# Optimization experiments

Hardware: AMD Instinct MI355X
Metric: run time of the kernel (lower is better)

The kernel has to match this reference:

```python
import jax, jax.numpy as jnp
import numpy as np

B, S, E, H, D = 4, 2048, 1024, 8, 128
EPS = 1e-5


def _ln(x, g, b):
    m = jnp.mean(x, axis=-1, keepdims=True)
    v = jnp.mean((x - m) ** 2, axis=-1, keepdims=True)
    return (x - m) * jax.lax.rsqrt(v + EPS) * g + b


def _xavier(k, shape, fan_in, fan_out):
    lim = float(np.sqrt(6.0 / (fan_in + fan_out)))
    return jax.random.uniform(k, shape, jnp.float32, -lim, lim)


def setup_inputs() -> dict:
    key = jax.random.key(0)
    ks = jax.random.split(key, 10)
    return {
        "x": jax.random.normal(ks[0], (B, S, E), jnp.float32),
        # embedding_to_z: Linear(E, H*D); stored as [E, H*D] for x @ W
        "W_ez": _xavier(ks[1], (E, H * D), E, H * D),
        "b_ez": jnp.zeros((H * D,), jnp.float32),
        "U_h": _xavier(ks[2], (H, D, D), D, D),
        "U_z": _xavier(ks[3], (H, D, D), D, D),
        "b_u": jnp.zeros((H, D), jnp.float32),
        "out_shaper": _xavier(ks[4], (H, D, D), D, D),
        # shared per-step state LayerNorm
        "lns_g": jnp.ones((D,), jnp.float32),
        "lns_b": jnp.zeros((D,), jnp.float32),
        # per-head FFN: LayerNorm(D) -> Linear(D,D) -> GELU -> Linear(D,E)
        "ff_ln_g": jnp.ones((H, D), jnp.float32),
        "ff_ln_b": jnp.zeros((H, D), jnp.float32),
        "ff_W1": _xavier(ks[5], (H, D, D), D, D),
        "ff_b1": jnp.zeros((H, D), jnp.float32),
        "ff_W2": _xavier(ks[6], (H, D, E), D, E),
        "ff_b2": jnp.zeros((H, E), jnp.float32),
        # layer_attention_weights: Linear(E, 1)
        "w_att": _xavier(ks[7], (E,), E, 1),
        "b_att": jnp.zeros((), jnp.float32),
        # output LayerNorm
        "lno_g": jnp.ones((E,), jnp.float32),
        "lno_b": jnp.zeros((E,), jnp.float32),
    }


def reference(x, W_ez, b_ez, U_h, U_z, b_u, out_shaper, lns_g, lns_b,
              ff_ln_g, ff_ln_b, ff_W1, ff_b1, ff_W2, ff_b2,
              w_att, b_att, lno_g, lno_b):
    b, s, _ = x.shape
    h, d = U_h.shape[0], U_h.shape[1]
    # z tokens: [B,S,H,D]
    z = jnp.tanh((x @ W_ez + b_ez).reshape(b, s, h, d))
    # torch.einsum('bhd,hdd->bhd') takes the DIAGONAL of the second operand
    uh_diag = jnp.einsum('hii->hi', U_h)          # [H,D]
    uz_diag = jnp.einsum('hii->hi', U_z)          # [H,D]
    os_diag = jnp.einsum('hii->hi', out_shaper)   # [H,D]

    def step(h_prev, z_t):
        # h_prev, z_t: [B,H,D]
        u = jax.nn.sigmoid(h_prev * uh_diag + z_t * uz_diag + b_u)
        h_new = u * h_prev + (1.0 - u) * z_t
        h_new = _ln(h_new, lns_g, lns_b)
        return h_new, h_new

    h0 = jnp.zeros((b, h, d), x.dtype)
    _, states = jax.lax.scan(step, h0, jnp.swapaxes(z, 0, 1))  # [S,B,H,D]
    states = jnp.swapaxes(states, 0, 1)                         # [B,S,H,D]

    shaped = states * os_diag                                   # diag einsum
    hln = _ln(shaped, ff_ln_g, ff_ln_b)                         # per-head LN
    h1 = jax.nn.gelu(jnp.einsum('bshd,hde->bshe', hln, ff_W1) + ff_b1,
                     approximate=False)                         # [B,S,H,D]
    ff_out = jnp.einsum('bshd,hde->bshe', h1, ff_W2) + ff_b2    # [B,S,H,E]

    scores = jax.nn.softmax(jnp.einsum('bshe,e->bsh', ff_out, w_att) + b_att,
                            axis=2)                             # over heads
    weighted = jnp.einsum('bshe,bsh->bse', ff_out, scores)      # [B,S,E]
    return _ln(weighted, lno_g, lno_b)
```

## Files before the change

kernel.cpp:

```cpp
#include <hip/hip_runtime.h>
#include <hip/hip_bf16.h>
#include <math.h>

#define BB 4
#define SS 2048
#define EE 1024
#define HH 8
#define DD 128
#define BSR (BB*SS)
#define HD  (HH*DD)
#define LNEPS 1e-5f
#define LOG2E 1.4426950408889634f

typedef __attribute__((ext_vector_type(8))) short bf16x8;
typedef __attribute__((ext_vector_type(4))) float f32x4;

__device__ __forceinline__ ushort f2bf(float f) {
    union { float f; unsigned u; } c{f};
    unsigned r = c.u + 0x7fff + ((c.u >> 16) & 1);
    return (ushort)(r >> 16);
}
__device__ __forceinline__ float bf2f(ushort b) {
    union { unsigned u; float f; } c{(unsigned)b << 16};
    return c.f;
}

typedef __attribute__((address_space(1))) const unsigned int GUI;
typedef __attribute__((address_space(3))) unsigned int LUI;
__device__ __forceinline__ void gl_lds16(const ushort* g, ushort* l) {
    __builtin_amdgcn_global_load_lds((GUI*)g, (LUI*)l, 16, 0, 0);
}

__global__ __launch_bounds__(256)
void prep_k(const float* __restrict__ W2, const float* __restrict__ w_att,
            const float* __restrict__ b2, const float* __restrict__ b_att,
            const float* __restrict__ Uh, const float* __restrict__ Uz,
            const float* __restrict__ Os,
            float* __restrict__ q, float* __restrict__ c,
            float* __restrict__ uh_d, float* __restrict__ uz_d,
            float* __restrict__ os_d)
{
    const int gid  = blockIdx.x * 256 + threadIdx.x;
    const int wave = gid >> 6, lane = gid & 63;
    if (wave < HD) {
        const float* wp = W2 + (size_t)wave * EE;
        float p = 0.f;
        for (int e = lane; e < EE; e += 64) p = fmaf(wp[e], w_att[e], p);
        #pragma unroll
        for (int off = 32; off > 0; off >>= 1) p += __shfl_xor(p, off, 64);
        if (lane == 0) {
            q[wave] = p;
            const int h = wave >> 7, d = wave & 127;
            uh_d[wave] = Uh[(size_t)h*DD*DD + (size_t)d*DD + d];
            uz_d[wave] = Uz[(size_t)h*DD*DD + (size_t)d*DD + d];
            os_d[wave] = Os[(size_t)h*DD*DD + (size_t)d*DD + d];
        }
    } else if (wave < HD + HH) {
        const int h = wave - HD;
        const float* bp = b2 + (size_t)h * EE;
        float p = 0.f;
        for (int e = lane; e < EE; e += 64) p = fmaf(bp[e], w_att[e], p);
        #pragma unroll
        for (int off = 32; off > 0; off >>= 1) p += __shfl_xor(p, off, 64);
        if (lane == 0) c[h] = p + b_att[0];
    }
}

__global__ __launch_bounds__(256)
void convx2_k(const float* __restrict__ x,
              ushort* __restrict__ hi, ushort* __restrict__ lo)
{
    const size_t idx = ((size_t)blockIdx.x * 256 + threadIdx.x) * 4;
    const float4 v = *(const float4*)(x + idx);
    ushort4 oh, ol;
    oh.x = f2bf(v.x); ol.x = f2bf(v.x - bf2f(oh.x));
    oh.y = f2bf(v.y); ol.y = f2bf(v.y - bf2f(oh.y));
    oh.z = f2bf(v.z); ol.z = f2bf(v.z - bf2f(oh.z));
    oh.w = f2bf(v.w); ol.w = f2bf(v.w - bf2f(oh.w));
    *(ushort4*)(hi + idx) = oh;
    *(ushort4*)(lo + idx) = ol;
}

__global__ __launch_bounds__(256)
void convT2_k(const float* __restrict__ W,
              ushort* __restrict__ Wth, ushort* __restrict__ Wtl)
{
    __shared__ float tile[32][33];
    const int k0 = blockIdx.x * 32, n0 = blockIdx.y * 32;
    const int tx = threadIdx.x & 31, ty = threadIdx.x >> 5;
    #pragma unroll
    for (int i = 0; i < 4; ++i)
        tile[ty + i*8][tx] = W[(size_t)(k0 + ty + i*8) * 1024 + n0 + tx];
    __syncthreads();
    #pragma unroll
    for (int i = 0; i < 4; ++i) {
        const float v = tile[tx][ty + i*8];
        const ushort h = f2bf(v);
        Wth[(size_t)(n0 + ty + i*8) * 1024 + k0 + tx] = h;
        Wtl[(size_t)(n0 + ty + i*8) * 1024 + k0 + tx] = f2bf(v - bf2f(h));
    }
}

__global__ __launch_bounds__(256)
void convT_k(const float* __restrict__ W, ushort* __restrict__ Wt)
{
    __shared__ float tile[32][33];
    const int k0 = blockIdx.x * 32, n0 = blockIdx.y * 32;
    const int tx = threadIdx.x & 31, ty = threadIdx.x >> 5;
    #pragma unroll
    for (int i = 0; i < 4; ++i)
        tile[ty + i*8][tx] = W[(size_t)(k0 + ty + i*8) * 1024 + n0 + tx];
    __syncthreads();
    #pragma unroll
    for (int i = 0; i < 4; ++i)
        Wt[(size_t)(n0 + ty + i*8) * 1024 + k0 + tx] = f2bf(tile[tx][ty + i*8]);
}

__global__ __launch_bounds__(256)
void gemm_mfma_hp(const ushort* __restrict__ Ah, const ushort* __restrict__ Al,
                  const ushort* __restrict__ Bh, const ushort* __restrict__ Bl,
                  float* __restrict__ C, const float* __restrict__ bias)
{
    __shared__ ushort AsmH[128*32], AsmL[128*32];
    __shared__ ushort BsmH[128*32], BsmL[128*32];
    const int t = threadIdx.x, lane = t & 63, w = t >> 6;
    const int wr = w >> 1, wc = w & 1;
    const int row0 = blockIdx.x * 128, col0 = blockIdx.y * 128;

    const int lr = lane >> 2;
    const int lc = (lane & 3) ^ (lr & 3);
    const size_t aoff0 = (size_t)(row0 +      w*16 + lr) * 1024 + lc*8;
    const size_t aoff1 = (size_t)(row0 + 64 + w*16 + lr) * 1024 + lc*8;
    const size_t boff0 = (size_t)(col0 +      w*16 + lr) * 1024 + lc*8;
    const size_t boff1 = (size_t)(col0 + 64 + w*16 + lr) * 1024 + lc*8;
    ushort* lds0 = (ushort*)nullptr;
    (void)lds0;
    ushort* AH0 = AsmH + (     w*16) * 32;  ushort* AH1 = AsmH + (64 + w*16) * 32;
    ushort* AL0 = AsmL + (     w*16) * 32;  ushort* AL1 = AsmL + (64 + w*16) * 32;
    ushort* BH0 = BsmH + (     w*16) * 32;  ushort* BH1 = BsmH + (64 + w*16) * 32;
    ushort* BL0 = BsmL + (     w*16) * 32;  ushort* BL1 = BsmL + (64 + w*16) * 32;

    f32x4 acc[4][4];
    #pragma unroll
    for (int i = 0; i < 4; ++i)
        #pragma unroll
        for (int j = 0; j < 4; ++j) acc[i][j] = (f32x4){0.f,0.f,0.f,0.f};

    const int quad = lane >> 4;
    const int fr   = lane & 15;
    const int fchk = (quad ^ (lane & 3)) * 8;

    for (int k0 = 0; k0 < 1024; k0 += 32) {
        __syncthreads();
        gl_lds16(Ah + aoff0 + k0, AH0);
        gl_lds16(Ah + aoff1 + k0, AH1);
        gl_lds16(Bh + boff0 + k0, BH0);
        gl_lds16(Bh + boff1 + k0, BH1);
        gl_lds16(Al + aoff0 + k0, AL0);
        gl_lds16(Al + aoff1 + k0, AL1);
        gl_lds16(Bl + boff0 + k0, BL0);
        gl_lds16(Bl + boff1 + k0, BL1);
        __syncthreads();

        bf16x8 afh[4], afl[4], bfh[4], bfl[4];
        #pragma unroll
        for (int i = 0; i < 4; ++i) {
            const int ra = (wr*64 + i*16 + fr) * 32 + fchk;
            afh[i] = *(const bf16x8*)(AsmH + ra);
            afl[i] = *(const bf16x8*)(AsmL + ra);
            const int rb = (wc*64 + i*16 + fr) * 32 + fchk;
            bfh[i] = *(const bf16x8*)(BsmH + rb);
            bfl[i] = *(const bf16x8*)(BsmL + rb);
        }
        #pragma unroll
        for (int i = 0; i < 4; ++i)
            #pragma unroll
            for (int j = 0; j < 4; ++j) {
                acc[i][j] = __builtin_amdgcn_mfma_f32_16x16x32_bf16(
                    afh[i], bfl[j], acc[i][j], 0, 0, 0);
                acc[i][j] = __builtin_amdgcn_mfma_f32_16x16x32_bf16(
                    afl[i], bfh[j], acc[i][j], 0, 0, 0);
                acc[i][j] = __builtin_amdgcn_mfma_f32_16x16x32_bf16(
                    afh[i], bfh[j], acc[i][j], 0, 0, 0);
            }
    }

    float colv[4];
    #pragma unroll
    for (int tj = 0; tj < 4; ++tj)
        colv[tj] = bias[col0 + wc*64 + tj*16 + fr];
    #pragma unroll
    for (int ti = 0; ti < 4; ++ti)
        #pragma unroll
        for (int i = 0; i < 4; ++i) {
            const int row = row0 + wr*64 + ti*16 + quad*4 + i;
            #pragma unroll
            for (int tj = 0; tj < 4; ++tj) {
                const int col = col0 + wc*64 + tj*16 + fr;
                C[(size_t)row*1024 + col] = tanhf(acc[ti][tj][i] + colv[tj]);
            }
        }
}

__global__ __launch_bounds__(256)
void gemm_mfma(const ushort* __restrict__ A, const ushort* __restrict__ Bt,
               float* __restrict__ C,
               const float* __restrict__ scores, const float* __restrict__ b2)
{
    __shared__ ushort Asm[128*32];
    __shared__ ushort Bsm[128*32];
    const int t = threadIdx.x, lane = t & 63, w = t >> 6;
    const int wr = w >> 1, wc = w & 1;
    const int row0 = blockIdx.x * 128, col0 = blockIdx.y * 128;

    const int lr = lane >> 2;
    const int lc = (lane & 3) ^ (lr & 3);
    const ushort* Ag0 = A  + (size_t)(row0 +      w*16 + lr) * 1024 + lc*8;
    const ushort* Ag1 = A  + (size_t)(row0 + 64 + w*16 + lr) * 1024 + lc*8;
    const ushort* Bg0 = Bt + (size_t)(col0 +      w*16 + lr) * 1024 + lc*8;
    const ushort* Bg1 = Bt + (size_t)(col0 + 64 + w*16 + lr) * 1024 + lc*8;
    ushort* Al0 = Asm + (     w*16) * 32;
    ushort* Al1 = Asm + (64 + w*16) * 32;
    ushort* Bl0 = Bsm + (     w*16) * 32;
    ushort* Bl1 = Bsm + (64 + w*16) * 32;

    f32x4 acc[4][4];
    #pragma unroll
    for (int i = 0; i < 4; ++i)
        #pragma unroll
        for (int j = 0; j < 4; ++j) acc[i][j] = (f32x4){0.f,0.f,0.f,0.f};

    const int quad = lane >> 4;
    const int fr   = lane & 15;
    const int fchk = (quad ^ (lane & 3)) * 8;

    for (int k0 = 0; k0 < 1024; k0 += 32) {
        __syncthreads();
        gl_lds16(Ag0 + k0, Al0);
        gl_lds16(Ag1 + k0, Al1);
        gl_lds16(Bg0 + k0, Bl0);
        gl_lds16(Bg1 + k0, Bl1);
        __syncthreads();

        bf16x8 af[4], bf[4];
        #pragma unroll
        for (int i = 0; i < 4; ++i) {
            af[i] = *(const bf16x8*)(Asm + (wr*64 + i*16 + fr)*32 + fchk);
            bf[i] = *(const bf16x8*)(Bsm + (wc*64 + i*16 + fr)*32 + fchk);
        }
        #pragma unroll
        for (int i = 0; i < 4; ++i)
            #pragma unroll
            for (int j = 0; j < 4; ++j)
                acc[i][j] = __builtin_amdgcn_mfma_f32_16x16x32_bf16(
                    af[i], bf[j], acc[i][j], 0, 0, 0);
    }

    float b2v[4][HH];
    #pragma unroll
    for (int tj = 0; tj < 4; ++tj) {
        const int col = col0 + wc*64 + tj*16 + fr;
        #pragma unroll
        for (int h = 0; h < HH; ++h) b2v[tj][h] = b2[(size_t)h*EE + col];
    }
    #pragma unroll
    for (int ti = 0; ti < 4; ++ti)
        #pragma unroll
        for (int i = 0; i < 4; ++i) {
            const int row = row0 + wr*64 + ti*16 + quad*4 + i;
            float sc[HH];
            #pragma unroll
            for (int h = 0; h < HH; ++h) sc[h] = scores[row*HH + h];
            #pragma unroll
            for (int tj = 0; tj < 4; ++tj) {
                const int col = col0 + wc*64 + tj*16 + fr;
                float bb = 0.f;
                #pragma unroll
                for (int h = 0; h < HH; ++h) bb = fmaf(sc[h], b2v[tj][h], bb);
                C[(size_t)row*1024 + col] = acc[ti][tj][i] + bb;
            }
        }
}

__global__ __launch_bounds__(256)
void gemm_k(const float* __restrict__ A, int lda, int aOff,
            const float* __restrict__ Bm, int ldb, int bOff,
            float* __restrict__ C, int ldc, int cOff,
            int K,
            const float* __restrict__ bias, int biasOff)
{
    const int zb = blockIdx.z;
    const float* Ab = A  + (size_t)zb * aOff;
    const float* Bb = Bm + (size_t)zb * bOff;
    float*       Cb = C  + (size_t)zb * cOff;
    const float* biasb = bias + (size_t)zb * biasOff;
    const int row0 = blockIdx.x * 128;
    const int col0 = blockIdx.y * 128;

    __shared__ float Asm[8][128];
    __shared__ float Bsm[8][128];

    const int t  = threadIdx.x;
    const int tx = t & 15, ty = t >> 4;
    const int am = t >> 1, ak = (t & 1) * 4;
    const int bk = t >> 5, bn = (t & 31) * 4;

    float acc[8][8];
    #pragma unroll
    for (int i = 0; i < 8; ++i)
        #pragma unroll
        for (int j = 0; j < 8; ++j) acc[i][j] = 0.f;

    for (int k0 = 0; k0 < K; k0 += 8) {
        const float4 av = *(const float4*)(Ab + (size_t)(row0 + am) * lda + k0 + ak);
        const float4 bv = *(const float4*)(Bb + (size_t)(k0 + bk) * ldb + col0 + bn);
        __syncthreads();
        Asm[ak+0][am] = av.x; Asm[ak+1][am] = av.y;
        Asm[ak+2][am] = av.z; Asm[ak+3][am] = av.w;
        *(float4*)&Bsm[bk][bn] = bv;
        __syncthreads();
        #pragma unroll
        for (int kk = 0; kk < 8; ++kk) {
            float a[8], b[8];
            *(float4*)&a[0] = *(const float4*)&Asm[kk][ty*8];
            *(float4*)&a[4] = *(const float4*)&Asm[kk][ty*8+4];
            *(float4*)&b[0] = *(const float4*)&Bsm[kk][tx*8];
            *(float4*)&b[4] = *(const float4*)&Bsm[kk][tx*8+4];
            #pragma unroll
            for (int i = 0; i < 8; ++i)
                #pragma unroll
                for (int j = 0; j < 8; ++j)
                    acc[i][j] = fmaf(a[i], b[j], acc[i][j]);
        }
    }

    #pragma unroll
    for (int i = 0; i < 8; ++i) {
        const int r = row0 + ty*8 + i;
        float outv[8];
        #pragma unroll
        for (int j = 0; j < 8; ++j) {
            const int cidx = col0 + tx*8 + j;
            float v = acc[i][j] + biasb[cidx];
            v = 0.5f * v * (1.f + erff(v * 0.70710678118654752f));
            outv[j] = v;
        }
        *(float4*)(Cb + (size_t)r*ldc + col0 + tx*8)     = *(float4*)&outv[0];
        *(float4*)(Cb + (size_t)r*ldc + col0 + tx*8 + 4) = *(float4*)&outv[4];
    }
}

__device__ __forceinline__ float dpp_add(float x, const int ctrl) {
    int y;
    switch (ctrl) {
        case 0x111: y = __builtin_amdgcn_update_dpp(0, __float_as_int(x), 0x111, 0xf, 0xf, true); break;
        case 0x112: y = __builtin_amdgcn_update_dpp(0, __float_as_int(x), 0x112, 0xf, 0xf, true); break;
        case 0x114: y = __builtin_amdgcn_update_dpp(0, __float_as_int(x), 0x114, 0xf, 0xf, true); break;
        case 0x118: y = __builtin_amdgcn_update_dpp(0, __float_as_int(x), 0x118, 0xf, 0xf, true); break;
        case 0x142: y = __builtin_amdgcn_update_dpp(0, __float_as_int(x), 0x142, 0xf, 0xf, true); break;
        default:    y = __builtin_amdgcn_update_dpp(0, __float_as_int(x), 0x143, 0xf, 0xf, true); break;
    }
    return x + __int_as_float(y);
}

__device__ __forceinline__ float wave_sum64(float x) {
    x = dpp_add(x, 0x111);
    x = dpp_add(x, 0x112);
    x = dpp_add(x, 0x114);
    x = dpp_add(x, 0x118);
    x = dpp_add(x, 0x142);
    x = dpp_add(x, 0x143);
    return __int_as_float(__builtin_amdgcn_readlane(__float_as_int(x), 63));
}

__global__ __launch_bounds__(64)
void scan_k(const float* __restrict__ z,
            const float* __restrict__ uh_d, const float* __restrict__ uz_d,
            const float* __restrict__ b_u,
            const float* __restrict__ lns_g, const float* __restrict__ lns_b,
            float* __restrict__ states)
{
    const int bh = blockIdx.x;
    const int b = bh >> 3, h = bh & 7;
    const int lane = threadIdx.x;
    const int d0 = lane, d1 = lane + 64;

    const float uhn0 = -uh_d[h*DD + d0] * LOG2E, uhn1 = -uh_d[h*DD + d1] * LOG2E;
    const float uzn0 = -uz_d[h*DD + d0] * LOG2E, uzn1 = -uz_d[h*DD + d1] * LOG2E;
    const float bun0 = -b_u [h*DD + d0] * LOG2E, bun1 = -b_u [h*DD + d1] * LOG2E;
    const float g0  = lns_g[d0], g1 = lns_g[d1];
    const float be0 = lns_b[d0], be1 = lns_b[d1];

    const float* zp = z      + ((size_t)b * SS * HH + h) * DD;
    float*       sp = states + ((size_t)b * SS * HH + h) * DD;

    float hp0 = 0.f, hp1 = 0.f;
    const int CH = 8;
    float zc0[CH], zc1[CH], pr0[CH], pr1[CH];
    #pragma unroll
    for (int i = 0; i < CH; ++i) {
        zc0[i] = zp[(size_t)i*HD + d0];
        zc1[i] = zp[(size_t)i*HD + d1];
    }
    #pragma unroll
    for (int i = 0; i < CH; ++i) {
        pr0[i] = fmaf(zc0[i], uzn0, bun0);
        pr1[i] = fmaf(zc1[i], uzn1, bun1);
    }

    for (int s0 = 0; s0 < SS; s0 += CH) {
        float zn0[CH], zn1[CH];
        if (s0 + CH < SS) {
            #pragma unroll
            for (int i = 0; i < CH; ++i) {
                zn0[i] = zp[(size_t)(s0+CH+i)*HD + d0];
                zn1[i] = zp[(size_t)(s0+CH+i)*HD + d1];
            }
        } else {
            #pragma unroll
            for (int i = 0; i < CH; ++i) { zn0[i] = 0.f; zn1[i] = 0.f; }
        }
        #pragma unroll
        for (int i = 0; i < CH; ++i) {
            const float z0 = zc0[i], z1 = zc1[i];
            const float e0 = __builtin_amdgcn_exp2f(fmaf(hp0, uhn0, pr0[i]));
            const float e1 = __builtin_amdgcn_exp2f(fmaf(hp1, uhn1, pr1[i]));
            const float d0v = hp0 - z0;
            const float d1v = hp1 - z1;
            const float u0 = __builtin_amdgcn_rcpf(1.f + e0);
            const float u1 = __builtin_amdgcn_rcpf(1.f + e1);
            const float hn0 = fmaf(u0, d0v, z0);
            const float hn1 = fmaf(u1, d1v, z1);
            const float s1 = wave_sum64(hn0 + hn1);
            const float s2 = wave_sum64(fmaf(hn0, hn0, hn1*hn1));
            const float m   = s1 * (1.f/128.f);
            const float var = fmaf(s2, 1.f/128.f, -m*m);
            const float r   = __builtin_amdgcn_rsqf(var + LNEPS);
            const float rg0 = r * g0, rg1 = r * g1;
            hp0 = fmaf(hn0 - m, rg0, be0);
            hp1 = fmaf(hn1 - m, rg1, be1);
            sp[(size_t)(s0+i)*HD + d0] = hp0;
            sp[(size_t)(s0+i)*HD + d1] = hp1;
        }
        #pragma unroll
        for (int i = 0; i < CH; ++i) {
            zc0[i] = zn0[i]; zc1[i] = zn1[i];
            pr0[i] = fmaf(zn0[i], uzn0, bun0);
            pr1[i] = fmaf(zn1[i], uzn1, bun1);
        }
    }
}

__global__ __launch_bounds__(256)
void headln_k(const float* __restrict__ states, const float* __restrict__ os_d,
              const float* __restrict__ ffg, const float* __restrict__ ffb,
              float* __restrict__ hln)
{
    const int gid  = blockIdx.x * 256 + threadIdx.x;
    const int row  = gid >> 6;
    const int lane = gid & 63;
    const int h = row & 7;
    const float* xp = states + (size_t)row * DD;
    const float x0 = xp[lane]      * os_d[h*DD + lane];
    const float x1 = xp[lane + 64] * os_d[h*DD + lane + 64];
    float s1 = x0 + x1;
    float s2 = fmaf(x0, x0, x1*x1);
    #pragma unroll
    for (int off = 32; off > 0; off >>= 1) {
        s1 += __shfl_xor(s1, off, 64);
        s2 += __shfl_xor(s2, off, 64);
    }
    const float m   = s1 * (1.f/128.f);
    const float var = fmaf(s2, 1.f/128.f, -m*m);
    const float r   = rsqrtf(var + LNEPS);
    float* op = hln + (size_t)row * DD;
    op[lane]      = fmaf((x0 - m)*r, ffg[h*DD + lane],      ffb[h*DD + lane]);
    op[lane + 64] = fmaf((x1 - m)*r, ffg[h*DD + lane + 64], ffb[h*DD + lane + 64]);
}

__global__ __launch_bounds__(256)
void logits_k(const float* __restrict__ h1, const float* __restrict__ q,
              const float* __restrict__ c, float* __restrict__ logits)
{
    const int gid  = blockIdx.x * 256 + threadIdx.x;
    const int row  = gid >> 6;
    const int lane = gid & 63;
    const int h = row & 7;
    const float* xp = h1 + (size_t)row * DD;
    float p = fmaf(xp[lane], q[h*DD + lane], xp[lane+64] * q[h*DD + lane + 64]);
    #pragma unroll
    for (int off = 32; off > 0; off >>= 1) p += __shfl_xor(p, off, 64);
    if (lane == 0) logits[row] = p + c[h];
}

__global__ __launch_bounds__(256)
void softscale_k(const float* __restrict__ h1, const float* __restrict__ logits,
                 ushort* __restrict__ gb, float* __restrict__ scores)
{
    const int gid = blockIdx.x * 256 + threadIdx.x;
    const size_t idx = (size_t)gid * 4;
    const int bs = (int)(idx >> 10);
    const int h  = (int)((idx >> 7) & 7);
    float l[8];
    float mx = -1e30f;
    #pragma unroll
    for (int i = 0; i < 8; ++i) { l[i] = logits[bs*8 + i]; mx = fmaxf(mx, l[i]); }
    float den = 0.f;
    #pragma unroll
    for (int i = 0; i < 8; ++i) den += __expf(l[i] - mx);
    const float sc = __expf(l[h] - mx) / den;
    float4 v = *(const float4*)(h1 + idx);
    ushort4 o;
    o.x = f2bf(v.x * sc); o.y = f2bf(v.y * sc);
    o.z = f2bf(v.z * sc); o.w = f2bf(v.w * sc);
    *(ushort4*)(gb + idx) = o;
    if ((idx & 127) == 0) scores[bs*8 + h] = sc;
}

__global__ __launch_bounds__(256)
void finalln_k(const float* __restrict__ w, const float* __restrict__ g,
               const float* __restrict__ b, float* __restrict__ out)
{
    const int row = blockIdx.x;
    const int t = threadIdx.x;
    const float* xp = w + (size_t)row * EE;
    const float4 v = *(const float4*)(xp + t*4);
    float s1 = v.x + v.y + v.z + v.w;
    float s2 = v.x*v.x + v.y*v.y + v.z*v.z + v.w*v.w;
    #pragma unroll
    for (int off = 32; off > 0; off >>= 1) {
        s1 += __shfl_xor(s1, off, 64);
        s2 += __shfl_xor(s2, off, 64);
    }
    __shared__ float r1[4], r2[4];
    if ((t & 63) == 0) { r1[t>>6] = s1; r2[t>>6] = s2; }
    __syncthreads();
    s1 = r1[0] + r1[1] + r1[2] + r1[3];
    s2 = r2[0] + r2[1] + r2[2] + r2[3];
    const float m   = s1 * (1.f/1024.f);
    const float var = fmaf(s2, 1.f/1024.f, -m*m);
    const float r   = rsqrtf(var + LNEPS);
    const float4 gv = *(const float4*)(g + t*4);
    const float4 bv = *(const float4*)(b + t*4);
    float4 o;
    o.x = fmaf((v.x - m)*r, gv.x, bv.x);
    o.y = fmaf((v.y - m)*r, gv.y, bv.y);
    o.z = fmaf((v.z - m)*r, gv.z, bv.z);
    o.w = fmaf((v.w - m)*r, gv.w, bv.w);
    *(float4*)(out + (size_t)row*EE + t*4) = o;
}

extern "C" void kernel_launch(void* const* d_in, const int* in_sizes, int n_in,
                              void* d_out, int out_size, void* d_ws, size_t ws_size,
                              hipStream_t stream)
{
    const float* x       = (const float*)d_in[0];
    const float* W_ez    = (const float*)d_in[1];
    const float* b_ez    = (const float*)d_in[2];
    const float* U_h     = (const float*)d_in[3];
    const float* U_z     = (const float*)d_in[4];
    const float* b_u     = (const float*)d_in[5];
    const float* outsh   = (const float*)d_in[6];
    const float* lns_g   = (const float*)d_in[7];
    const float* lns_b   = (const float*)d_in[8];
    const float* ff_ln_g = (const float*)d_in[9];
    const float* ff_ln_b = (const float*)d_in[10];
    const float* ff_W1   = (const float*)d_in[11];
    const float* ff_b1   = (const float*)d_in[12];
    const float* ff_W2   = (const float*)d_in[13];
    const float* ff_b2   = (const float*)d_in[14];
    const float* w_att   = (const float*)d_in[15];
    const float* b_att   = (const float*)d_in[16];
    const float* lno_g   = (const float*)d_in[17];
    const float* lno_b   = (const float*)d_in[18];
    float* out = (float*)d_out;

    float* ws = (float*)d_ws;
    const size_t NBIG = (size_t)BSR * HD;
    float* bufA = ws;
    float* bufB = ws + NBIG;
    float* bufC = ws + 2*NBIG;
    float* ext  = ws + 3*NBIG;
    ushort* W2t   = (ushort*)ext;
    float* logits = ext + 512*1024;
    float* scores = logits + BSR*HH;
    float* qv     = scores + BSR*HH;
    float* cv     = qv + HD;
    float* uh_d   = cv + 8;
    float* uz_d   = uh_d + HD;
    float* os_d   = uz_d + HD;
    ushort* xb_hi = (ushort*)bufB;
    ushort* xb_lo = (ushort*)bufB + NBIG;
    ushort* gb    = (ushort*)bufB;
    ushort* WezT_hi = (ushort*)bufC;
    ushort* WezT_lo = (ushort*)bufC + 1024*1024;

    convx2_k<<<(BSR*EE/4)/256, 256, 0, stream>>>(x, xb_hi, xb_lo);
    convT2_k<<<dim3(32, 32), 256, 0, stream>>>(W_ez, WezT_hi, WezT_lo);
    convT_k<<<dim3(32, 32), 256, 0, stream>>>(ff_W2, W2t);
    prep_k<<<258, 256, 0, stream>>>(ff_W2, w_att, ff_b2, b_att,
                                    U_h, U_z, outsh, qv, cv, uh_d, uz_d, os_d);
    gemm_mfma_hp<<<dim3(64, 8), 256, 0, stream>>>(
        xb_hi, xb_lo, WezT_hi, WezT_lo, bufA, b_ez);
    scan_k<<<BB*HH, 64, 0, stream>>>(bufA, uh_d, uz_d, b_u, lns_g, lns_b, bufB);
    headln_k<<<(BSR*HH*64)/256, 256, 0, stream>>>(bufB, os_d, ff_ln_g, ff_ln_b, bufC);
    gemm_k<<<dim3(64, 1, 8), 256, 0, stream>>>(
        bufC, HD, DD, ff_W1, DD, DD*DD, bufA, HD, DD, DD, ff_b1, DD);
    logits_k<<<(BSR*HH*64)/256, 256, 0, stream>>>(bufA, qv, cv, logits);
    softscale_k<<<(BSR*HD/4)/256, 256, 0, stream>>>(bufA, logits, gb, scores);
    gemm_mfma<<<dim3(64, 8), 256, 0, stream>>>(gb, W2t, bufC, scores, ff_b2);
    finalln_k<<<BSR, 256, 0, stream>>>(bufC, lno_g, lno_b, out);
}
```

Measured before the change: 648.8 us.

## Fuse head LayerNorm into scan and use bf16 MFMA for first FFN GEMM

```diff
diff --git a/kernel.cpp b/kernel.cpp
--- a/kernel.cpp
+++ b/kernel.cpp
@@ -117,6 +117,24 @@
 }
 
 __global__ __launch_bounds__(256)
+void convTH_k(const float* __restrict__ W, ushort* __restrict__ Wt)
+{
+    __shared__ float tile[32][33];
+    const int hh = blockIdx.z;
+    const int k0 = blockIdx.x * 32, n0 = blockIdx.y * 32;
+    const int tx = threadIdx.x & 31, ty = threadIdx.x >> 5;
+    const float* Wb = W + (size_t)hh * DD * DD;
+    ushort*      Wtb = Wt + (size_t)hh * DD * DD;
+    #pragma unroll
+    for (int i = 0; i < 4; ++i)
+        tile[ty + i*8][tx] = Wb[(size_t)(k0 + ty + i*8) * DD + n0 + tx];
+    __syncthreads();
+    #pragma unroll
+    for (int i = 0; i < 4; ++i)
+        Wtb[(size_t)(n0 + ty + i*8) * DD + k0 + tx] = f2bf(tile[tx][ty + i*8]);
+}
+
+__global__ __launch_bounds__(256)
 void gemm_mfma_hp(const ushort* __restrict__ Ah, const ushort* __restrict__ Al,
                   const ushort* __restrict__ Bh, const ushort* __restrict__ Bl,
                   float* __restrict__ C, const float* __restrict__ bias)
@@ -133,8 +151,6 @@
     const size_t aoff1 = (size_t)(row0 + 64 + w*16 + lr) * 1024 + lc*8;
     const size_t boff0 = (size_t)(col0 +      w*16 + lr) * 1024 + lc*8;
     const size_t boff1 = (size_t)(col0 + 64 + w*16 + lr) * 1024 + lc*8;
-    ushort* lds0 = (ushort*)nullptr;
-    (void)lds0;
     ushort* AH0 = AsmH + (     w*16) * 32;  ushort* AH1 = AsmH + (64 + w*16) * 32;
     ushort* AL0 = AsmL + (     w*16) * 32;  ushort* AL1 = AsmL + (64 + w*16) * 32;
     ushort* BH0 = BsmH + (     w*16) * 32;  ushort* BH1 = BsmH + (64 + w*16) * 32;
@@ -283,71 +299,76 @@
 }
 
 __global__ __launch_bounds__(256)
-void gemm_k(const float* __restrict__ A, int lda, int aOff,
-            const float* __restrict__ Bm, int ldb, int bOff,
-            float* __restrict__ C, int ldc, int cOff,
-            int K,
-            const float* __restrict__ bias, int biasOff)
-{
-    const int zb = blockIdx.z;
-    const float* Ab = A  + (size_t)zb * aOff;
-    const float* Bb = Bm + (size_t)zb * bOff;
-    float*       Cb = C  + (size_t)zb * cOff;
-    const float* biasb = bias + (size_t)zb * biasOff;
+void gemm_h1(const ushort* __restrict__ A, const ushort* __restrict__ Bt,
+             const float* __restrict__ b1, float* __restrict__ C)
+{
+    const int hh = blockIdx.z;
+    __shared__ ushort Asm[128*32];
+    __shared__ ushort Bsm[128*32];
+    const int t = threadIdx.x, lane = t & 63, w = t >> 6;
+    const int wr = w >> 1, wc = w & 1;
     const int row0 = blockIdx.x * 128;
-    const int col0 = blockIdx.y * 128;
-
-    __shared__ float Asm[8][128];
-    __shared__ float Bsm[8][128];
-
-    const int t  = threadIdx.x;
-    const int tx = t & 15, ty = t >> 4;
-    const int am = t >> 1, ak = (t & 1) * 4;
-    const int bk = t >> 5, bn = (t & 31) * 4;
-
-    float acc[8][8];
-    #pragma unroll
-    for (int i = 0; i < 8; ++i)
-        #pragma unroll
-        for (int j = 0; j < 8; ++j) acc[i][j] = 0.f;
-
-    for (int k0 = 0; k0 < K; k0 += 8) {
-        const float4 av = *(const float4*)(Ab + (size_t)(row0 + am) * lda + k0 + ak);
-        const float4 bv = *(const float4*)(Bb + (size_t)(k0 + bk) * ldb + col0 + bn);
+
+    const int lr = lane >> 2;
+    const int lc = (lane & 3) ^ (lr & 3);
+    const ushort* Ag0 = A + (size_t)(row0 +      w*16 + lr) * 1024 + hh*DD + lc*8;
+    const ushort* Ag1 = A + (size_t)(row0 + 64 + w*16 + lr) * 1024 + hh*DD + lc*8;
+    const ushort* Bg0 = Bt + (size_t)hh*DD*DD + (     w*16 + lr) * DD + lc*8;
+    const ushort* Bg1 = Bt + (size_t)hh*DD*DD + (64 + w*16 + lr) * DD + lc*8;
+    ushort* Al0 = Asm + (     w*16) * 32;
+    ushort* Al1 = Asm + (64 + w*16) * 32;
+    ushort* Bl0 = Bsm + (     w*16) * 32;
+    ushort* Bl1 = Bsm + (64 + w*16) * 32;
+
+    f32x4 acc[4][4];
+    #pragma unroll
+    for (int i = 0; i < 4; ++i)
+        #pragma unroll
+        for (int j = 0; j < 4; ++j) acc[i][j] = (f32x4){0.f,0.f,0.f,0.f};
+
+    const int quad = lane >> 4;
+    const int fr   = lane & 15;
+    const int fchk = (quad ^ (lane & 3)) * 8;
+
+    for (int k0 = 0; k0 < 128; k0 += 32) {
         __syncthreads();
-        Asm[ak+0][am] = av.x; Asm[ak+1][am] = av.y;
-        Asm[ak+2][am] = av.z; Asm[ak+3][am] = av.w;
-        *(float4*)&Bsm[bk][bn] = bv;
+        gl_lds16(Ag0 + k0, Al0);
+        gl_lds16(Ag1 + k0, Al1);
+        gl_lds16(Bg0 + k0, Bl0);
+        gl_lds16(Bg1 + k0, Bl1);
         __syncthreads();
-        #pragma unroll
-        for (int kk = 0; kk < 8; ++kk) {
-            float a[8], b[8];
-            *(float4*)&a[0] = *(const float4*)&Asm[kk][ty*8];
-            *(float4*)&a[4] = *(const float4*)&Asm[kk][ty*8+4];
-            *(float4*)&b[0] = *(const float4*)&Bsm[kk][tx*8];
-            *(float4*)&b[4] = *(const float4*)&Bsm[kk][tx*8+4];
-            #pragma unroll
-            for (int i = 0; i < 8; ++i)
-                #pragma unroll
-                for (int j = 0; j < 8; ++j)
-                    acc[i][j] = fmaf(a[i], b[j], acc[i][j]);
-        }
-    }
-
-    #pragma unroll
-    for (int i = 0; i < 8; ++i) {
-        const int r = row0 + ty*8 + i;
-        float outv[8];
-        #pragma unroll
-        for (int j = 0; j < 8; ++j) {
-            const int cidx = col0 + tx*8 + j;
-            float v = acc[i][j] + biasb[cidx];
-            v = 0.5f * v * (1.f + erff(v * 0.70710678118654752f));
-            outv[j] = v;
-        }
-        *(float4*)(Cb + (size_t)r*ldc + col0 + tx*8)     = *(float4*)&outv[0];
-        *(float4*)(Cb + (size_t)r*ldc + col0 + tx*8 + 4) = *(float4*)&outv[4];
-    }
+
+        bf16x8 af[4], bf[4];
+        #pragma unroll
+        for (int i = 0; i < 4; ++i) {
+            af[i] = *(const bf16x8*)(Asm + (wr*64 + i*16 + fr)*32 + fchk);
+            bf[i] = *(const bf16x8*)(Bsm + (wc*64 + i*16 + fr)*32 + fchk);
+        }
+        #pragma unroll
+        for (int i = 0; i < 4; ++i)
+            #pragma unroll
+            for (int j = 0; j < 4; ++j)
+                acc[i][j] = __builtin_amdgcn_mfma_f32_16x16x32_bf16(
+                    af[i], bf[j], acc[i][j], 0, 0, 0);
+    }
+
+    float colv[4];
+    #pragma unroll
+    for (int tj = 0; tj < 4; ++tj)
+        colv[tj] = b1[hh*DD + wc*64 + tj*16 + fr];
+    #pragma unroll
+    for (int ti = 0; ti < 4; ++ti)
+        #pragma unroll
+        for (int i = 0; i < 4; ++i) {
+            const int row = row0 + wr*64 + ti*16 + quad*4 + i;
+            #pragma unroll
+            for (int tj = 0; tj < 4; ++tj) {
+                const int col = wc*64 + tj*16 + fr;
+                float v = acc[ti][tj][i] + colv[tj];
+                v = 0.5f * v * (1.f + erff(v * 0.70710678118654752f));
+                C[(size_t)row*1024 + hh*DD + col] = v;
+            }
+        }
 }
 
 __device__ __forceinline__ float dpp_add(float x, const int ctrl) {
@@ -378,59 +399,58 @@
             const float* __restrict__ uh_d, const float* __restrict__ uz_d,
             const float* __restrict__ b_u,
             const float* __restrict__ lns_g, const float* __restrict__ lns_b,
-            float* __restrict__ states)
+            const float* __restrict__ os_d,
+            const float* __restrict__ ffg, const float* __restrict__ ffb,
+            ushort* __restrict__ hln)
 {
     const int bh = blockIdx.x;
     const int b = bh >> 3, h = bh & 7;
-    const int lane = threadIdx.x;
-    const int d0 = lane, d1 = lane + 64;
-
-    const float uhn0 = -uh_d[h*DD + d0] * LOG2E, uhn1 = -uh_d[h*DD + d1] * LOG2E;
-    const float uzn0 = -uz_d[h*DD + d0] * LOG2E, uzn1 = -uz_d[h*DD + d1] * LOG2E;
-    const float bun0 = -b_u [h*DD + d0] * LOG2E, bun1 = -b_u [h*DD + d1] * LOG2E;
+    const int l = threadIdx.x;
+    const int d0 = 2*l, d1 = d0 + 1;
+
+    const float uhn0 = -uh_d[h*DD+d0] * LOG2E, uhn1 = -uh_d[h*DD+d1] * LOG2E;
+    const float uzn0 = -uz_d[h*DD+d0] * LOG2E, uzn1 = -uz_d[h*DD+d1] * LOG2E;
+    const float bun0 = -b_u [h*DD+d0] * LOG2E, bun1 = -b_u [h*DD+d1] * LOG2E;
     const float g0  = lns_g[d0], g1 = lns_g[d1];
     const float be0 = lns_b[d0], be1 = lns_b[d1];
-
-    const float* zp = z      + ((size_t)b * SS * HH + h) * DD;
-    float*       sp = states + ((size_t)b * SS * HH + h) * DD;
+    const float os0 = os_d[h*DD+d0], os1 = os_d[h*DD+d1];
+    const float fg0 = ffg[h*DD+d0],  fg1 = ffg[h*DD+d1];
+    const float fb0 = ffb[h*DD+d0],  fb1 = ffb[h*DD+d1];
+
+    const float* zp = z + ((size_t)b * SS * HH + h) * DD + d0;
+    unsigned* op = (unsigned*)(hln + (size_t)b * SS * HD + h * DD) + l;
 
     float hp0 = 0.f, hp1 = 0.f;
     const int CH = 8;
-    float zc0[CH], zc1[CH], pr0[CH], pr1[CH];
+    float2 zc[CH]; float pb0[CH], pb1[CH];
+    #pragma unroll
+    for (int i = 0; i < CH; ++i) zc[i] = *(const float2*)(zp + (size_t)i*HD);
     #pragma unroll
     for (int i = 0; i < CH; ++i) {
-        zc0[i] = zp[(size_t)i*HD + d0];
-        zc1[i] = zp[(size_t)i*HD + d1];
-    }
-    #pragma unroll
-    for (int i = 0; i < CH; ++i) {
-        pr0[i] = fmaf(zc0[i], uzn0, bun0);
-        pr1[i] = fmaf(zc1[i], uzn1, bun1);
+        pb0[i] = fmaf(zc[i].x, uzn0, bun0);
+        pb1[i] = fmaf(zc[i].y, uzn1, bun1);
     }
 
     for (int s0 = 0; s0 < SS; s0 += CH) {
-        float zn0[CH], zn1[CH];
+        float2 zn[CH];
         if (s0 + CH < SS) {
             #pragma unroll
-            for (int i = 0; i < CH; ++i) {
-                zn0[i] = zp[(size_t)(s0+CH+i)*HD + d0];
-                zn1[i] = zp[(size_t)(s0+CH+i)*HD + d1];
-            }
+            for (int i = 0; i < CH; ++i)
+                zn[i] = *(const float2*)(zp + (size_t)(s0+CH+i)*HD);
         } else {
             #pragma unroll
-            for (int i = 0; i < CH; ++i) { zn0[i] = 0.f; zn1[i] = 0.f; }
+            for (int i = 0; i < CH; ++i) zn[i] = make_float2(0.f, 0.f);
         }
         #pragma unroll
         for (int i = 0; i < CH; ++i) {
-            const float z0 = zc0[i], z1 = zc1[i];
-            const float e0 = __builtin_amdgcn_exp2f(fmaf(hp0, uhn0, pr0[i]));
-            const float e1 = __builtin_amdgcn_exp2f(fmaf(hp1, uhn1, pr1[i]));
-            const float d0v = hp0 - z0;
-            const float d1v = hp1 - z1;
+            const float z0 = zc[i].x, z1 = zc[i].y;
+            const float e0 = __builtin_amdgcn_exp2f(fmaf(hp0, uhn0, pb0[i]));
+            const float e1 = __builtin_amdgcn_exp2f(fmaf(hp1, uhn1, pb1[i]));
+            const float dv0 = hp0 - z0, dv1 = hp1 - z1;
             const float u0 = __builtin_amdgcn_rcpf(1.f + e0);
             const float u1 = __builtin_amdgcn_rcpf(1.f + e1);
-            const float hn0 = fmaf(u0, d0v, z0);
-            const float hn1 = fmaf(u1, d1v, z1);
+            const float hn0 = fmaf(u0, dv0, z0);
+            const float hn1 = fmaf(u1, dv1, z1);
             const float s1 = wave_sum64(hn0 + hn1);
             const float s2 = wave_sum64(fmaf(hn0, hn0, hn1*hn1));
             const float m   = s1 * (1.f/128.f);
@@ -439,43 +459,24 @@
             const float rg0 = r * g0, rg1 = r * g1;
             hp0 = fmaf(hn0 - m, rg0, be0);
             hp1 = fmaf(hn1 - m, rg1, be1);
-            sp[(size_t)(s0+i)*HD + d0] = hp0;
-            sp[(size_t)(s0+i)*HD + d1] = hp1;
+            const float y0 = hp0 * os0, y1 = hp1 * os1;
+            const float t1 = wave_sum64(y0 + y1);
+            const float t2 = wave_sum64(fmaf(y0, y0, y1*y1));
+            const float my = t1 * (1.f/128.f);
+            const float vy = fmaf(t2, 1.f/128.f, -my*my);
+            const float ry = __builtin_amdgcn_rsqf(vy + LNEPS);
+            const float o0 = fmaf(y0 - my, ry * fg0, fb0);
+            const float o1 = fmaf(y1 - my, ry * fg1, fb1);
+            op[(size_t)(s0+i) * (HD/2)] =
+                (unsigned)f2bf(o0) | ((unsigned)f2bf(o1) << 16);
         }
         #pragma unroll
         for (int i = 0; i < CH; ++i) {
-            zc0[i] = zn0[i]; zc1[i] = zn1[i];
-            pr0[i] = fmaf(zn0[i], uzn0, bun0);
-            pr1[i] = fmaf(zn1[i], uzn1, bun1);
-        }
-    }
-}
-
-__global__ __launch_bounds__(256)
-void headln_k(const float* __restrict__ states, const float* __restrict__ os_d,
-              const float* __restrict__ ffg, const float* __restrict__ ffb,
-              float* __restrict__ hln)
-{
-    const int gid  = blockIdx.x * 256 + threadIdx.x;
-    const int row  = gid >> 6;
-    const int lane = gid & 63;
-    const int h = row & 7;
-    const float* xp = states + (size_t)row * DD;
-    const float x0 = xp[lane]      * os_d[h*DD + lane];
-    const float x1 = xp[lane + 64] * os_d[h*DD + lane + 64];
-    float s1 = x0 + x1;
-    float s2 = fmaf(x0, x0, x1*x1);
-    #pragma unroll
-    for (int off = 32; off > 0; off >>= 1) {
-        s1 += __shfl_xor(s1, off, 64);
-        s2 += __shfl_xor(s2, off, 64);
-    }
-    const float m   = s1 * (1.f/128.f);
-    const float var = fmaf(s2, 1.f/128.f, -m*m);
-    const float r   = rsqrtf(var + LNEPS);
-    float* op = hln + (size_t)row * DD;
-    op[lane]      = fmaf((x0 - m)*r, ffg[h*DD + lane],      ffb[h*DD + lane]);
-    op[lane + 64] = fmaf((x1 - m)*r, ffg[h*DD + lane + 64], ffb[h*DD + lane + 64]);
+            zc[i] = zn[i];
+            pb0[i] = fmaf(zn[i].x, uzn0, bun0);
+            pb1[i] = fmaf(zn[i].y, uzn1, bun1);
+        }
+    }
 }
 
 __global__ __launch_bounds__(256)
@@ -582,7 +583,8 @@
     float* bufC = ws + 2*NBIG;
     float* ext  = ws + 3*NBIG;
     ushort* W2t   = (ushort*)ext;
-    float* logits = ext + 512*1024;
+    ushort* W1t   = (ushort*)(ext + 512*1024);
+    float* logits = ext + 512*1024 + 64*1024;
     float* scores = logits + BSR*HH;
     float* qv     = scores + BSR*HH;
     float* cv     = qv + HD;
@@ -591,23 +593,26 @@
     float* os_d   = uz_d + HD;
     ushort* xb_hi = (ushort*)bufB;
     ushort* xb_lo = (ushort*)bufB + NBIG;
-    ushort* gb    = (ushort*)bufB;
+    ushort* hlnb  = (ushort*)bufB;
+    float*  wsum  = bufB;
     ushort* WezT_hi = (ushort*)bufC;
     ushort* WezT_lo = (ushort*)bufC + 1024*1024;
+    float*  h1f   = bufC;
+    ushort* gb    = (ushort*)bufA;
 
     convx2_k<<<(BSR*EE/4)/256, 256, 0, stream>>>(x, xb_hi, xb_lo);
     convT2_k<<<dim3(32, 32), 256, 0, stream>>>(W_ez, WezT_hi, WezT_lo);
     convT_k<<<dim3(32, 32), 256, 0, stream>>>(ff_W2, W2t);
+    convTH_k<<<dim3(4, 4, 8), 256, 0, stream>>>(ff_W1, W1t);
     prep_k<<<258, 256, 0, stream>>>(ff_W2, w_att, ff_b2, b_att,
                                     U_h, U_z, outsh, qv, cv, uh_d, uz_d, os_d);
     gemm_mfma_hp<<<dim3(64, 8), 256, 0, stream>>>(
         xb_hi, xb_lo, WezT_hi, WezT_lo, bufA, b_ez);
-    scan_k<<<BB*HH, 64, 0, stream>>>(bufA, uh_d, uz_d, b_u, lns_g, lns_b, bufB);
-    headln_k<<<(BSR*HH*64)/256, 256, 0, stream>>>(bufB, os_d, ff_ln_g, ff_ln_b, bufC);
-    gemm_k<<<dim3(64, 1, 8), 256, 0, stream>>>(
-        bufC, HD, DD, ff_W1, DD, DD*DD, bufA, HD, DD, DD, ff_b1, DD);
-    logits_k<<<(BSR*HH*64)/256, 256, 0, stream>>>(bufA, qv, cv, logits);
-    softscale_k<<<(BSR*HD/4)/256, 256, 0, stream>>>(bufA, logits, gb, scores);
-    gemm_mfma<<<dim3(64, 8), 256, 0, stream>>>(gb, W2t, bufC, scores, ff_b2);
-    finalln_k<<<BSR, 256, 0, stream>>>(bufC, lno_g, lno_b, out);
-}
+    scan_k<<<BB*HH, 64, 0, stream>>>(bufA, uh_d, uz_d, b_u, lns_g, lns_b,
+                                     os_d, ff_ln_g, ff_ln_b, hlnb);
+    gemm_h1<<<dim3(64, 1, 8), 256, 0, stream>>>(hlnb, W1t, ff_b1, h1f);
+    logits_k<<<(BSR*HH*64)/256, 256, 0, stream>>>(h1f, qv, cv, logits);
+    softscale_k<<<(BSR*HD/4)/256, 256, 0, stream>>>(h1f, logits, gb, scores);
+    gemm_mfma<<<dim3(64, 8), 256, 0, stream>>>(gb, W2t, wsum, scores, ff_b2);
+    finalln_k<<<BSR, 256, 0, stream>>>(wsum, lno_g, lno_b, out);
+}
```

New measurement: 727.0 us. 1.12x slower.
